# Performance work log

Hardware: AMD Instinct MI355X
Metric: run time of the kernel (lower is better)

Reference implementation:

```python
import jax, jax.numpy as jnp
import numpy as np
import math

VOCAB = 32000
D_MODEL = 64
N_LAYERS = 4
B, S = 512, 1000
EPS = 1e-5


def _layer_norm(x, g, b):
    mu = jnp.mean(x, axis=-1, keepdims=True)
    var = jnp.mean(jnp.square(x - mu), axis=-1, keepdims=True)
    return (x - mu) * jax.lax.rsqrt(var + EPS) * g + b


def _pos_encoding(seq_len, d_model, dtype):
    pos = jnp.arange(seq_len, dtype=dtype)[:, None]                      # [S,1]
    div = jnp.exp(jnp.arange(0, d_model, 2, dtype=dtype) * (-math.log(10000.0) / d_model))  # [d/2]
    ang = pos * div                                                       # [S,d/2]
    pe = jnp.stack([jnp.sin(ang), jnp.cos(ang)], axis=-1).reshape(seq_len, d_model)
    return pe  # [S,d]


def setup_inputs() -> dict:
    key = jax.random.key(0)
    ks = jax.random.split(key, 14)
    d, L = D_MODEL, N_LAYERS
    sc = 0.05
    return {
        "tokens": jax.random.randint(ks[0], (B, S), 0, VOCAB, dtype=jnp.int64 if jax.config.jax_enable_x64 else jnp.int32),
        "emb":   jax.random.normal(ks[1], (VOCAB, d), jnp.float32) * sc,
        "lin_w": jax.random.normal(ks[2], (L, d, d), jnp.float32) * sc,   # [out,in] per layer
        "lin_b": jnp.zeros((L, d), jnp.float32),
        "ff1_w": jax.random.normal(ks[3], (L, d, d), jnp.float32) * sc,
        "ff1_b": jnp.zeros((L, d), jnp.float32),
        "ff2_w": jax.random.normal(ks[4], (L, d, d), jnp.float32) * sc,
        "ff2_b": jnp.zeros((L, d), jnp.float32),
        "n1_g":  jnp.ones((L, d), jnp.float32),
        "n1_b":  jnp.zeros((L, d), jnp.float32),
        "n2_g":  jnp.ones((L, d), jnp.float32),
        "n2_b":  jnp.zeros((L, d), jnp.float32),
        "out_w": jax.random.normal(ks[5], (2, d), jnp.float32) * sc,
        "out_b": jnp.zeros((2,), jnp.float32),
    }


def reference(tokens, emb, lin_w, lin_b, ff1_w, ff1_b, ff2_w, ff2_b,
              n1_g, n1_b, n2_g, n2_b, out_w, out_b):
    d = emb.shape[1]
    x = emb[tokens] * jnp.asarray(math.sqrt(d), emb.dtype)               # [B,S,d]
    x = x + _pos_encoding(tokens.shape[1], d, x.dtype)[None, :, :]
    # dropout is identity in eval mode
    for l in range(lin_w.shape[0]):
        avg = jnp.mean(x, axis=1, keepdims=True)                          # [B,1,d]
        attn = jnp.einsum('bkd,od->bko', avg, lin_w[l]) + lin_b[l]        # [B,1,d], broadcasts
        x = _layer_norm(x + attn, n1_g[l], n1_b[l])
        h = jax.nn.relu(jnp.einsum('bsd,od->bso', x, ff1_w[l]) + ff1_b[l])
        h = jnp.einsum('bsd,od->bso', h, ff2_w[l]) + ff2_b[l]
        x = _layer_norm(x + h, n2_g[l], n2_b[l])
    logits = jnp.einsum('bsd,od->bso', x, out_w) + out_b                  # [B,S,2]
    return logits
```

## Files before the change

### kernel.cpp

```cpp
#include <hip/hip_runtime.h>
#include <stdint.h>

#define TPB 1024
#define NL 4

typedef _Float16 f16;
typedef _Float16 half2v __attribute__((ext_vector_type(2)));
typedef _Float16 f16x8 __attribute__((ext_vector_type(8)));
typedef float f32x4 __attribute__((ext_vector_type(4)));
typedef uint32_t u32x2 __attribute__((ext_vector_type(2)));
typedef uint32_t u32x4 __attribute__((ext_vector_type(4)));

#define XIU(r, c) ((r) * 32 + (((((c) >> 2) ^ ((r) & 7))) << 2) + ((c) & 3))

static __device__ __forceinline__ uint32_t packh2(float a, float b) {
  half2v h;
  h.x = (_Float16)a;
  h.y = (_Float16)b;
  return __builtin_bit_cast(uint32_t, h);
}
static __device__ __forceinline__ float2 unpackh2(uint32_t u) {
  half2v h = __builtin_bit_cast(half2v, u);
  return make_float2((float)h.x, (float)h.y);
}

__global__ void pack_weights_kernel(const float* __restrict__ ff1_w,
                                    const float* __restrict__ ff2_w,
                                    f16* __restrict__ w1h,
                                    f16* __restrict__ w2h,
                                    float* __restrict__ petab) {
  int idx = blockIdx.x * blockDim.x + threadIdx.x;
  if (idx < 16384) {
    w1h[idx] = (f16)ff1_w[idx];
  } else if (idx < 32768) {
    w2h[idx - 16384] = (f16)ff2_w[idx - 16384];
  } else if (petab != nullptr && idx < 32768 + 64000) {
    int j = idx - 32768;
    int s = j >> 6, d = j & 63;
    float div = exp2f(-0.4152410118609203f * (float)(d >> 1));
    float ang = (float)s * div;
    petab[j] = (d & 1) ? cosf(ang) : sinf(ang);
  }
}

__global__ __launch_bounds__(TPB) void aat_kernel(
    const int* __restrict__ tokens, const float* __restrict__ emb,
    const float* __restrict__ lin_w, const float* __restrict__ lin_b,
    const float* __restrict__ ff1_b, const float* __restrict__ ff2_b,
    const float* __restrict__ n1_g, const float* __restrict__ n1_b,
    const float* __restrict__ n2_g, const float* __restrict__ n2_b,
    const float* __restrict__ out_w, const float* __restrict__ out_b,
    const f16* __restrict__ w1h, const f16* __restrict__ w2h,
    const float* __restrict__ petab, float* __restrict__ out) {
  __shared__ __align__(16) uint32_t X2[1024 * 32];
  __shared__ __align__(16) uint32_t Hreg[256 * 32];

  const int t = threadIdx.x;
  const int b = blockIdx.x;
  const int lane = t & 63;
  const int wv = t >> 6;
  const bool valid = (t < 1000);
  float* redbuf = (float*)Hreg;
  float* avgbuf = (float*)(Hreg + 2048);
  float* attnbuf = (float*)(Hreg + 2112);

  if (valid) {
    int tok = tokens[b * 1000 + t];
    const float4* ev = (const float4*)(emb + (size_t)tok * 64);
    const int r7 = t & 7;
    if (petab != nullptr) {
      const float4* pv = (const float4*)(petab + (size_t)t * 64);
      #pragma unroll
      for (int q = 0; q < 8; q++) {
        float4 v0 = ev[2 * q], v1 = ev[2 * q + 1];
        float4 p0 = pv[2 * q], p1 = pv[2 * q + 1];
        u32x4 w;
        w[0] = packh2(fmaf(v0.x, 8.f, p0.x), fmaf(v0.y, 8.f, p0.y));
        w[1] = packh2(fmaf(v0.z, 8.f, p0.z), fmaf(v0.w, 8.f, p0.w));
        w[2] = packh2(fmaf(v1.x, 8.f, p1.x), fmaf(v1.y, 8.f, p1.y));
        w[3] = packh2(fmaf(v1.z, 8.f, p1.z), fmaf(v1.w, 8.f, p1.w));
        *(u32x4*)(&X2[t * 32 + ((q ^ r7) << 2)]) = w;
      }
    } else {
      float fs = (float)t;
      #pragma unroll
      for (int q = 0; q < 8; q++) {
        float4 v0 = ev[2 * q], v1 = ev[2 * q + 1];
        float d0 = exp2f(-0.4152410118609203f * (float)(4 * q));
        float d1 = exp2f(-0.4152410118609203f * (float)(4 * q + 1));
        float d2 = exp2f(-0.4152410118609203f * (float)(4 * q + 2));
        float d3 = exp2f(-0.4152410118609203f * (float)(4 * q + 3));
        u32x4 w;
        w[0] = packh2(fmaf(v0.x, 8.f, sinf(fs * d0)), fmaf(v0.y, 8.f, cosf(fs * d0)));
        w[1] = packh2(fmaf(v0.z, 8.f, sinf(fs * d1)), fmaf(v0.w, 8.f, cosf(fs * d1)));
        w[2] = packh2(fmaf(v1.x, 8.f, sinf(fs * d2)), fmaf(v1.y, 8.f, cosf(fs * d2)));
        w[3] = packh2(fmaf(v1.z, 8.f, sinf(fs * d3)), fmaf(v1.w, 8.f, cosf(fs * d3)));
        *(u32x4*)(&X2[t * 32 + ((q ^ r7) << 2)]) = w;
      }
    }
  } else {
    #pragma unroll
    for (int c = 0; c < 32; c += 4)
      *(u32x4*)(&X2[t * 32 + c]) = (u32x4){0u, 0u, 0u, 0u};
  }
  __syncthreads();

  const int l15 = lane & 15;
  const int g4 = lane >> 4;
  const int e7 = l15 & 7;
  const int nt = wv & 3;
  const int mr = wv >> 2;
  const int cw = 8 * nt + 2 * g4;
  const int cswz = (((cw >> 2) ^ e7) << 2) + (cw & 3);

  #pragma unroll 1
  for (int l = 0; l < NL; l++) {
    const float* n1g = n1_g + l * 64;
    const float* n1b = n1_b + l * 64;
    const float* n2gl = n2_g + l * 64;
    const float* n2bl = n2_b + l * 64;

    const f16* w1p = w1h + l * 4096 + (16 * nt + l15) * 64 + 8 * g4;
    f16x8 A10 = *(const f16x8*)(w1p);
    f16x8 A11 = *(const f16x8*)(w1p + 32);
    const f16* w2p = w2h + l * 4096 + (16 * nt + l15) * 64 + 8 * g4;
    f16x8 A20 = *(const f16x8*)(w2p);
    f16x8 A21 = *(const f16x8*)(w2p + 32);
    f32x4 bias1 = *(const f32x4*)(ff1_b + l * 64 + 16 * nt + 4 * g4);
    f32x4 bias2 = *(const f32x4*)(ff2_b + l * 64 + 16 * nt + 4 * g4);

    {
      int cp = t & 31, rg = t >> 5;
      float s0 = 0.f, s1 = 0.f;
      for (int r = rg; r < 1000; r += 32) {
        float2 v = unpackh2(X2[XIU(r, cp)]);
        s0 += v.x;
        s1 += v.y;
      }
      redbuf[rg * 64 + 2 * cp] = s0;
      redbuf[rg * 64 + 2 * cp + 1] = s1;
    }
    __syncthreads();
    if (t < 64) {
      float ssum = 0.f;
      #pragma unroll
      for (int w = 0; w < 32; w++) ssum += redbuf[w * 64 + t];
      avgbuf[t] = ssum * 1e-3f;
    }
    if (t < 64) {
      const float* wr = lin_w + (size_t)(l * 64 + t) * 64;
      float a0 = lin_b[l * 64 + t], a1 = 0.f, a2 = 0.f, a3 = 0.f;
      #pragma unroll
      for (int d = 0; d < 64; d += 4) {
        a0 += avgbuf[d] * wr[d];
        a1 += avgbuf[d + 1] * wr[d + 1];
        a2 += avgbuf[d + 2] * wr[d + 2];
        a3 += avgbuf[d + 3] * wr[d + 3];
      }
      attnbuf[t] = (a0 + a1) + (a2 + a3);
    }
    __syncthreads();

    if (valid) {
      const float2* at2 = (const float2*)attnbuf;
      const int r7 = t & 7;
      float m0 = 0.f, q0 = 0.f;
      #pragma unroll
      for (int q = 0; q < 8; q++) {
        u32x4 w = *(const u32x4*)(&X2[t * 32 + ((q ^ r7) << 2)]);
        #pragma unroll
        for (int j = 0; j < 4; j++) {
          float2 xv = unpackh2(w[j]);
          float2 at = at2[q * 4 + j];
          float a0 = xv.x + at.x, a1 = xv.y + at.y;
          m0 += a0 + a1;
          q0 = fmaf(a0, a0, q0);
          q0 = fmaf(a1, a1, q0);
        }
      }
      float mu = m0 * (1.0f / 64.0f);
      float var = q0 * (1.0f / 64.0f) - mu * mu;
      float rs = rsqrtf(var + 1e-5f);
      #pragma unroll
      for (int q = 0; q < 8; q++) {
        u32x4 w = *(const u32x4*)(&X2[t * 32 + ((q ^ r7) << 2)]);
        u32x4 o;
        #pragma unroll
        for (int j = 0; j < 4; j++) {
          float2 xv = unpackh2(w[j]);
          float2 at = at2[q * 4 + j];
          int d = (q * 4 + j) * 2;
          float a0 = xv.x + at.x, a1 = xv.y + at.y;
          o[j] = packh2(fmaf((a0 - mu) * rs, n1g[d], n1b[d]),
                        fmaf((a1 - mu) * rs, n1g[d + 1], n1b[d + 1]));
        }
        *(u32x4*)(&X2[t * 32 + ((q ^ r7) << 2)]) = o;
      }
    }
    __syncthreads();

    #pragma unroll 1
    for (int i = 0; i < 4; i++) {
      const int s0 = 256 * i + 64 * mr;
      #pragma unroll 2
      for (int sb = 0; sb < 4; sb++) {
        const int s = s0 + 16 * sb + l15;
        u32x4 b0 = *(const u32x4*)(&X2[s * 32 + ((g4 ^ e7) << 2)]);
        u32x4 b1 = *(const u32x4*)(&X2[s * 32 + (((4 + g4) ^ e7) << 2)]);
        f32x4 acc = bias1;
        acc = __builtin_amdgcn_mfma_f32_16x16x32_f16(
            A10, __builtin_bit_cast(f16x8, b0), acc, 0, 0, 0);
        acc = __builtin_amdgcn_mfma_f32_16x16x32_f16(
            A11, __builtin_bit_cast(f16x8, b1), acc, 0, 0, 0);
        const int hr = 64 * mr + 16 * sb + l15;
        u32x2 hp;
        hp[0] = packh2(fmaxf(acc[0], 0.f), fmaxf(acc[1], 0.f));
        hp[1] = packh2(fmaxf(acc[2], 0.f), fmaxf(acc[3], 0.f));
        *(u32x2*)(&Hreg[hr * 32 + cswz]) = hp;
      }
      __syncthreads();
      #pragma unroll 2
      for (int sb = 0; sb < 4; sb++) {
        const int s = s0 + 16 * sb + l15;
        const int hr = 64 * mr + 16 * sb + l15;
        u32x4 h0 = *(const u32x4*)(&Hreg[hr * 32 + ((g4 ^ e7) << 2)]);
        u32x4 h1 = *(const u32x4*)(&Hreg[hr * 32 + (((4 + g4) ^ e7) << 2)]);
        u32x2 ry = *(const u32x2*)(&X2[s * 32 + cswz]);
        float2 r0 = unpackh2(ry[0]), r1 = unpackh2(ry[1]);
        f32x4 acc = bias2;
        acc[0] += r0.x;
        acc[1] += r0.y;
        acc[2] += r1.x;
        acc[3] += r1.y;
        acc = __builtin_amdgcn_mfma_f32_16x16x32_f16(
            A20, __builtin_bit_cast(f16x8, h0), acc, 0, 0, 0);
        acc = __builtin_amdgcn_mfma_f32_16x16x32_f16(
            A21, __builtin_bit_cast(f16x8, h1), acc, 0, 0, 0);
        u32x2 tw;
        tw[0] = packh2(acc[0], acc[1]);
        tw[1] = packh2(acc[2], acc[3]);
        *(u32x2*)(&X2[s * 32 + cswz]) = tw;
      }
      __syncthreads();
    }

    if (valid) {
      const int r7 = t & 7;
      float m0 = 0.f, q0 = 0.f;
      #pragma unroll
      for (int q = 0; q < 8; q++) {
        u32x4 w = *(const u32x4*)(&X2[t * 32 + ((q ^ r7) << 2)]);
        #pragma unroll
        for (int j = 0; j < 4; j++) {
          float2 tv = unpackh2(w[j]);
          m0 += tv.x + tv.y;
          q0 = fmaf(tv.x, tv.x, q0);
          q0 = fmaf(tv.y, tv.y, q0);
        }
      }
      float mu2 = m0 * (1.0f / 64.0f);
      float var2 = q0 * (1.0f / 64.0f) - mu2 * mu2;
      float rs2 = rsqrtf(var2 + 1e-5f);
      #pragma unroll
      for (int q = 0; q < 8; q++) {
        u32x4 w = *(const u32x4*)(&X2[t * 32 + ((q ^ r7) << 2)]);
        u32x4 o;
        #pragma unroll
        for (int j = 0; j < 4; j++) {
          float2 tv = unpackh2(w[j]);
          int d = (q * 4 + j) * 2;
          o[j] = packh2(fmaf((tv.x - mu2) * rs2, n2gl[d], n2bl[d]),
                        fmaf((tv.y - mu2) * rs2, n2gl[d + 1], n2bl[d + 1]));
        }
        *(u32x4*)(&X2[t * 32 + ((q ^ r7) << 2)]) = o;
      }
    } else {
      #pragma unroll
      for (int c = 0; c < 32; c += 4)
        *(u32x4*)(&X2[t * 32 + c]) = (u32x4){0u, 0u, 0u, 0u};
    }
    __syncthreads();
  }

  if (valid) {
    const int r7 = t & 7;
    float a0 = out_b[0], a1 = out_b[1];
    #pragma unroll
    for (int q = 0; q < 8; q++) {
      u32x4 w = *(const u32x4*)(&X2[t * 32 + ((q ^ r7) << 2)]);
      #pragma unroll
      for (int j = 0; j < 4; j++) {
        float2 xv = unpackh2(w[j]);
        int d = (q * 4 + j) * 2;
        a0 += xv.x * out_w[d] + xv.y * out_w[d + 1];
        a1 += xv.x * out_w[64 + d] + xv.y * out_w[64 + d + 1];
      }
    }
    *(float2*)(out + (size_t)(b * 1000 + t) * 2) = make_float2(a0, a1);
  }
}

extern "C" void kernel_launch(void* const* d_in, const int* in_sizes, int n_in,
                              void* d_out, int out_size, void* d_ws, size_t ws_size,
                              hipStream_t stream) {
  const int* tokens = (const int*)d_in[0];
  const float* emb = (const float*)d_in[1];
  const float* lin_w = (const float*)d_in[2];
  const float* lin_b = (const float*)d_in[3];
  const float* ff1_w = (const float*)d_in[4];
  const float* ff1_b = (const float*)d_in[5];
  const float* ff2_w = (const float*)d_in[6];
  const float* ff2_b = (const float*)d_in[7];
  const float* n1_g = (const float*)d_in[8];
  const float* n1_b = (const float*)d_in[9];
  const float* n2_g = (const float*)d_in[10];
  const float* n2_b = (const float*)d_in[11];
  const float* out_w = (const float*)d_in[12];
  const float* out_b = (const float*)d_in[13];
  float* out = (float*)d_out;

  f16* w1h = (f16*)d_ws;
  f16* w2h = w1h + 16384;
  float* petab = (float*)((char*)d_ws + 65536);
  const size_t need = 65536 + 64000 * 4;
  const bool use_pe = (ws_size >= need);
  float* pe_arg = use_pe ? petab : nullptr;

  int pack_threads = 32768 + (use_pe ? 64000 : 0);
  int pack_blocks = (pack_threads + 255) / 256;
  pack_weights_kernel<<<pack_blocks, 256, 0, stream>>>(ff1_w, ff2_w, w1h, w2h, pe_arg);
  aat_kernel<<<512, TPB, 0, stream>>>(tokens, emb, lin_w, lin_b, ff1_b, ff2_b,
                                      n1_g, n1_b, n2_g, n2_b, out_w, out_b,
                                      w1h, w2h, pe_arg, out);
}
```

Baseline: 280.8 us.

## Double-buffer FFN hidden tile to overlap GEMM1 and GEMM2 with fewer barriers

Splits the FFN over 1024 rows into 8 chunks of 128 rows and double-buffers the hidden activations in shared memory. The first GEMM of chunk c now runs alongside the second GEMM of chunk c-1, with a single barrier per chunk instead of two per 256-row slab. The layer-norm passes also keep the row in registers instead of re-reading shared memory. This adds register pressure and a scheduling barrier, and the row mapping changes per wave.

Result: slower. 309.1 us (+10.1%).

```diff
diff --git a/kernel.cpp b/kernel.cpp
--- a/kernel.cpp
+++ b/kernel.cpp
@@ -53,16 +53,16 @@
     const f16* __restrict__ w1h, const f16* __restrict__ w2h,
     const float* __restrict__ petab, float* __restrict__ out) {
   __shared__ __align__(16) uint32_t X2[1024 * 32];
-  __shared__ __align__(16) uint32_t Hreg[256 * 32];
+  __shared__ __align__(16) uint32_t Hb[2 * 4096];
 
   const int t = threadIdx.x;
   const int b = blockIdx.x;
   const int lane = t & 63;
   const int wv = t >> 6;
   const bool valid = (t < 1000);
-  float* redbuf = (float*)Hreg;
-  float* avgbuf = (float*)(Hreg + 2048);
-  float* attnbuf = (float*)(Hreg + 2112);
+  float* redbuf = (float*)Hb;
+  float* avgbuf = (float*)(Hb + 2048);
+  float* attnbuf = (float*)(Hb + 2112);
 
   if (valid) {
     int tok = tokens[b * 1000 + t];
@@ -164,116 +164,111 @@
     if (valid) {
       const float2* at2 = (const float2*)attnbuf;
       const int r7 = t & 7;
+      u32x4 wq0 = *(const u32x4*)(&X2[t * 32 + ((0 ^ r7) << 2)]);
+      u32x4 wq1 = *(const u32x4*)(&X2[t * 32 + ((1 ^ r7) << 2)]);
+      u32x4 wq2 = *(const u32x4*)(&X2[t * 32 + ((2 ^ r7) << 2)]);
+      u32x4 wq3 = *(const u32x4*)(&X2[t * 32 + ((3 ^ r7) << 2)]);
+      u32x4 wq4 = *(const u32x4*)(&X2[t * 32 + ((4 ^ r7) << 2)]);
+      u32x4 wq5 = *(const u32x4*)(&X2[t * 32 + ((5 ^ r7) << 2)]);
+      u32x4 wq6 = *(const u32x4*)(&X2[t * 32 + ((6 ^ r7) << 2)]);
+      u32x4 wq7 = *(const u32x4*)(&X2[t * 32 + ((7 ^ r7) << 2)]);
       float m0 = 0.f, q0 = 0.f;
-      #pragma unroll
-      for (int q = 0; q < 8; q++) {
-        u32x4 w = *(const u32x4*)(&X2[t * 32 + ((q ^ r7) << 2)]);
-        #pragma unroll
-        for (int j = 0; j < 4; j++) {
-          float2 xv = unpackh2(w[j]);
-          float2 at = at2[q * 4 + j];
-          float a0 = xv.x + at.x, a1 = xv.y + at.y;
-          m0 += a0 + a1;
-          q0 = fmaf(a0, a0, q0);
-          q0 = fmaf(a1, a1, q0);
-        }
-      }
+#define LN1S(WQ, Q) { _Pragma("unroll") for (int j = 0; j < 4; j++) { \
+      float2 xv = unpackh2(WQ[j]); float2 at = at2[(Q) * 4 + j]; \
+      float a0 = xv.x + at.x, a1 = xv.y + at.y; \
+      m0 += a0 + a1; q0 = fmaf(a0, a0, q0); q0 = fmaf(a1, a1, q0); } }
+      LN1S(wq0, 0) LN1S(wq1, 1) LN1S(wq2, 2) LN1S(wq3, 3)
+      LN1S(wq4, 4) LN1S(wq5, 5) LN1S(wq6, 6) LN1S(wq7, 7)
+#undef LN1S
       float mu = m0 * (1.0f / 64.0f);
       float var = q0 * (1.0f / 64.0f) - mu * mu;
       float rs = rsqrtf(var + 1e-5f);
-      #pragma unroll
-      for (int q = 0; q < 8; q++) {
-        u32x4 w = *(const u32x4*)(&X2[t * 32 + ((q ^ r7) << 2)]);
-        u32x4 o;
-        #pragma unroll
-        for (int j = 0; j < 4; j++) {
-          float2 xv = unpackh2(w[j]);
-          float2 at = at2[q * 4 + j];
-          int d = (q * 4 + j) * 2;
-          float a0 = xv.x + at.x, a1 = xv.y + at.y;
-          o[j] = packh2(fmaf((a0 - mu) * rs, n1g[d], n1b[d]),
-                        fmaf((a1 - mu) * rs, n1g[d + 1], n1b[d + 1]));
-        }
-        *(u32x4*)(&X2[t * 32 + ((q ^ r7) << 2)]) = o;
-      }
-    }
-    __syncthreads();
-
+#define LN1N(WQ, Q) { u32x4 o; _Pragma("unroll") for (int j = 0; j < 4; j++) { \
+      float2 xv = unpackh2(WQ[j]); float2 at = at2[(Q) * 4 + j]; \
+      int d = ((Q) * 4 + j) * 2; \
+      float a0 = xv.x + at.x, a1 = xv.y + at.y; \
+      o[j] = packh2(fmaf((a0 - mu) * rs, n1g[d], n1b[d]), \
+                    fmaf((a1 - mu) * rs, n1g[d + 1], n1b[d + 1])); } \
+      *(u32x4*)(&X2[t * 32 + (((Q) ^ r7) << 2)]) = o; }
+      LN1N(wq0, 0) LN1N(wq1, 1) LN1N(wq2, 2) LN1N(wq3, 3)
+      LN1N(wq4, 4) LN1N(wq5, 5) LN1N(wq6, 6) LN1N(wq7, 7)
+#undef LN1N
+    }
+    __syncthreads();
+
+#define MM1C(C, HB) { _Pragma("unroll") for (int sb = 0; sb < 2; sb++) { \
+    const int s = 128 * (C) + 32 * mr + 16 * sb + l15; \
+    u32x4 b0 = *(const u32x4*)(&X2[s * 32 + ((g4 ^ e7) << 2)]); \
+    u32x4 b1 = *(const u32x4*)(&X2[s * 32 + (((4 + g4) ^ e7) << 2)]); \
+    f32x4 acc = bias1; \
+    acc = __builtin_amdgcn_mfma_f32_16x16x32_f16(A10, __builtin_bit_cast(f16x8, b0), acc, 0, 0, 0); \
+    acc = __builtin_amdgcn_mfma_f32_16x16x32_f16(A11, __builtin_bit_cast(f16x8, b1), acc, 0, 0, 0); \
+    const int hr = 32 * mr + 16 * sb + l15; \
+    u32x2 hp; \
+    hp[0] = packh2(fmaxf(acc[0], 0.f), fmaxf(acc[1], 0.f)); \
+    hp[1] = packh2(fmaxf(acc[2], 0.f), fmaxf(acc[3], 0.f)); \
+    *(u32x2*)(&(HB)[hr * 32 + cswz]) = hp; } }
+
+#define MM2C(C, HB) { _Pragma("unroll") for (int sb = 0; sb < 2; sb++) { \
+    const int s = 128 * (C) + 32 * mr + 16 * sb + l15; \
+    const int hr = 32 * mr + 16 * sb + l15; \
+    u32x4 h0 = *(const u32x4*)(&(HB)[hr * 32 + ((g4 ^ e7) << 2)]); \
+    u32x4 h1 = *(const u32x4*)(&(HB)[hr * 32 + (((4 + g4) ^ e7) << 2)]); \
+    u32x2 ry = *(const u32x2*)(&X2[s * 32 + cswz]); \
+    float2 r0 = unpackh2(ry[0]), r1 = unpackh2(ry[1]); \
+    f32x4 acc = bias2; \
+    acc[0] += r0.x; acc[1] += r0.y; acc[2] += r1.x; acc[3] += r1.y; \
+    acc = __builtin_amdgcn_mfma_f32_16x16x32_f16(A20, __builtin_bit_cast(f16x8, h0), acc, 0, 0, 0); \
+    acc = __builtin_amdgcn_mfma_f32_16x16x32_f16(A21, __builtin_bit_cast(f16x8, h1), acc, 0, 0, 0); \
+    u32x2 tw; \
+    tw[0] = packh2(acc[0], acc[1]); \
+    tw[1] = packh2(acc[2], acc[3]); \
+    *(u32x2*)(&X2[s * 32 + cswz]) = tw; } }
+
+    MM1C(0, Hb)
+    __syncthreads();
     #pragma unroll 1
-    for (int i = 0; i < 4; i++) {
-      const int s0 = 256 * i + 64 * mr;
-      #pragma unroll 2
-      for (int sb = 0; sb < 4; sb++) {
-        const int s = s0 + 16 * sb + l15;
-        u32x4 b0 = *(const u32x4*)(&X2[s * 32 + ((g4 ^ e7) << 2)]);
-        u32x4 b1 = *(const u32x4*)(&X2[s * 32 + (((4 + g4) ^ e7) << 2)]);
-        f32x4 acc = bias1;
-        acc = __builtin_amdgcn_mfma_f32_16x16x32_f16(
-            A10, __builtin_bit_cast(f16x8, b0), acc, 0, 0, 0);
-        acc = __builtin_amdgcn_mfma_f32_16x16x32_f16(
-            A11, __builtin_bit_cast(f16x8, b1), acc, 0, 0, 0);
-        const int hr = 64 * mr + 16 * sb + l15;
-        u32x2 hp;
-        hp[0] = packh2(fmaxf(acc[0], 0.f), fmaxf(acc[1], 0.f));
-        hp[1] = packh2(fmaxf(acc[2], 0.f), fmaxf(acc[3], 0.f));
-        *(u32x2*)(&Hreg[hr * 32 + cswz]) = hp;
-      }
+    for (int c = 1; c < 8; c++) {
+      uint32_t* cur = Hb + ((c & 1) << 12);
+      uint32_t* prv = Hb + (((c - 1) & 1) << 12);
+      MM1C(c, cur)
+      __builtin_amdgcn_sched_barrier(0);
+      MM2C(c - 1, prv)
       __syncthreads();
-      #pragma unroll 2
-      for (int sb = 0; sb < 4; sb++) {
-        const int s = s0 + 16 * sb + l15;
-        const int hr = 64 * mr + 16 * sb + l15;
-        u32x4 h0 = *(const u32x4*)(&Hreg[hr * 32 + ((g4 ^ e7) << 2)]);
-        u32x4 h1 = *(const u32x4*)(&Hreg[hr * 32 + (((4 + g4) ^ e7) << 2)]);
-        u32x2 ry = *(const u32x2*)(&X2[s * 32 + cswz]);
-        float2 r0 = unpackh2(ry[0]), r1 = unpackh2(ry[1]);
-        f32x4 acc = bias2;
-        acc[0] += r0.x;
-        acc[1] += r0.y;
-        acc[2] += r1.x;
-        acc[3] += r1.y;
-        acc = __builtin_amdgcn_mfma_f32_16x16x32_f16(
-            A20, __builtin_bit_cast(f16x8, h0), acc, 0, 0, 0);
-        acc = __builtin_amdgcn_mfma_f32_16x16x32_f16(
-            A21, __builtin_bit_cast(f16x8, h1), acc, 0, 0, 0);
-        u32x2 tw;
-        tw[0] = packh2(acc[0], acc[1]);
-        tw[1] = packh2(acc[2], acc[3]);
-        *(u32x2*)(&X2[s * 32 + cswz]) = tw;
-      }
-      __syncthreads();
-    }
+    }
+    MM2C(7, Hb + 4096)
+    __syncthreads();
+#undef MM1C
+#undef MM2C
 
     if (valid) {
       const int r7 = t & 7;
+      u32x4 wq0 = *(const u32x4*)(&X2[t * 32 + ((0 ^ r7) << 2)]);
+      u32x4 wq1 = *(const u32x4*)(&X2[t * 32 + ((1 ^ r7) << 2)]);
+      u32x4 wq2 = *(const u32x4*)(&X2[t * 32 + ((2 ^ r7) << 2)]);
+      u32x4 wq3 = *(const u32x4*)(&X2[t * 32 + ((3 ^ r7) << 2)]);
+      u32x4 wq4 = *(const u32x4*)(&X2[t * 32 + ((4 ^ r7) << 2)]);
+      u32x4 wq5 = *(const u32x4*)(&X2[t * 32 + ((5 ^ r7) << 2)]);
+      u32x4 wq6 = *(const u32x4*)(&X2[t * 32 + ((6 ^ r7) << 2)]);
+      u32x4 wq7 = *(const u32x4*)(&X2[t * 32 + ((7 ^ r7) << 2)]);
       float m0 = 0.f, q0 = 0.f;
-      #pragma unroll
-      for (int q = 0; q < 8; q++) {
-        u32x4 w = *(const u32x4*)(&X2[t * 32 + ((q ^ r7) << 2)]);
-        #pragma unroll
-        for (int j = 0; j < 4; j++) {
-          float2 tv = unpackh2(w[j]);
-          m0 += tv.x + tv.y;
-          q0 = fmaf(tv.x, tv.x, q0);
-          q0 = fmaf(tv.y, tv.y, q0);
-        }
-      }
+#define LN2S(WQ) { _Pragma("unroll") for (int j = 0; j < 4; j++) { \
+      float2 tv = unpackh2(WQ[j]); \
+      m0 += tv.x + tv.y; q0 = fmaf(tv.x, tv.x, q0); q0 = fmaf(tv.y, tv.y, q0); } }
+      LN2S(wq0) LN2S(wq1) LN2S(wq2) LN2S(wq3)
+      LN2S(wq4) LN2S(wq5) LN2S(wq6) LN2S(wq7)
+#undef LN2S
       float mu2 = m0 * (1.0f / 64.0f);
       float var2 = q0 * (1.0f / 64.0f) - mu2 * mu2;
       float rs2 = rsqrtf(var2 + 1e-5f);
-      #pragma unroll
-      for (int q = 0; q < 8; q++) {
-        u32x4 w = *(const u32x4*)(&X2[t * 32 + ((q ^ r7) << 2)]);
-        u32x4 o;
-        #pragma unroll
-        for (int j = 0; j < 4; j++) {
-          float2 tv = unpackh2(w[j]);
-          int d = (q * 4 + j) * 2;
-          o[j] = packh2(fmaf((tv.x - mu2) * rs2, n2gl[d], n2bl[d]),
-                        fmaf((tv.y - mu2) * rs2, n2gl[d + 1], n2bl[d + 1]));
-        }
-        *(u32x4*)(&X2[t * 32 + ((q ^ r7) << 2)]) = o;
-      }
+#define LN2N(WQ, Q) { u32x4 o; _Pragma("unroll") for (int j = 0; j < 4; j++) { \
+      float2 tv = unpackh2(WQ[j]); int d = ((Q) * 4 + j) * 2; \
+      o[j] = packh2(fmaf((tv.x - mu2) * rs2, n2gl[d], n2bl[d]), \
+                    fmaf((tv.y - mu2) * rs2, n2gl[d + 1], n2bl[d + 1])); } \
+      *(u32x4*)(&X2[t * 32 + (((Q) ^ r7) << 2)]) = o; }
+      LN2N(wq0, 0) LN2N(wq1, 1) LN2N(wq2, 2) LN2N(wq3, 3)
+      LN2N(wq4, 4) LN2N(wq5, 5) LN2N(wq6, 6) LN2N(wq7, 7)
+#undef LN2N
     } else {
       #pragma unroll
       for (int c = 0; c < 32; c += 4)
```

## Double-buffer hidden activations to overlap FF1 and FF2 across sequence chunks

Applied to the files above, without the earlier changes.

Replaces the four-chunk FF1/FF2 loop, which needed two barriers per chunk, with eight smaller 128-row chunks using two ping-pong H buffers. Each iteration computes FF1 for chunk c and FF2 for chunk c-1 with a single barrier between iterations, halving barrier count per chunk and letting MFMA work from the two stages interleave. Shared memory use stays the same size, but each MFMA phase now has less work per barrier, and a sched_barrier restricts compiler reordering.

New measurement: 280.9 us. About the same (+0.0%).

```diff
diff --git a/kernel.cpp b/kernel.cpp
--- a/kernel.cpp
+++ b/kernel.cpp
@@ -53,16 +53,16 @@
     const f16* __restrict__ w1h, const f16* __restrict__ w2h,
     const float* __restrict__ petab, float* __restrict__ out) {
   __shared__ __align__(16) uint32_t X2[1024 * 32];
-  __shared__ __align__(16) uint32_t Hreg[256 * 32];
+  __shared__ __align__(16) uint32_t Hb[2 * 4096];
 
   const int t = threadIdx.x;
   const int b = blockIdx.x;
   const int lane = t & 63;
   const int wv = t >> 6;
   const bool valid = (t < 1000);
-  float* redbuf = (float*)Hreg;
-  float* avgbuf = (float*)(Hreg + 2048);
-  float* attnbuf = (float*)(Hreg + 2112);
+  float* redbuf = (float*)Hb;
+  float* avgbuf = (float*)(Hb + 2048);
+  float* attnbuf = (float*)(Hb + 2112);
 
   if (valid) {
     int tok = tokens[b * 1000 + t];
@@ -199,50 +199,50 @@
     }
     __syncthreads();
 
+#define MM1C(C, HB) { _Pragma("unroll") for (int sb = 0; sb < 2; sb++) { \
+    const int s = 128 * (C) + 32 * mr + 16 * sb + l15; \
+    u32x4 b0 = *(const u32x4*)(&X2[s * 32 + ((g4 ^ e7) << 2)]); \
+    u32x4 b1 = *(const u32x4*)(&X2[s * 32 + (((4 + g4) ^ e7) << 2)]); \
+    f32x4 acc = bias1; \
+    acc = __builtin_amdgcn_mfma_f32_16x16x32_f16(A10, __builtin_bit_cast(f16x8, b0), acc, 0, 0, 0); \
+    acc = __builtin_amdgcn_mfma_f32_16x16x32_f16(A11, __builtin_bit_cast(f16x8, b1), acc, 0, 0, 0); \
+    const int hr = 32 * mr + 16 * sb + l15; \
+    u32x2 hp; \
+    hp[0] = packh2(fmaxf(acc[0], 0.f), fmaxf(acc[1], 0.f)); \
+    hp[1] = packh2(fmaxf(acc[2], 0.f), fmaxf(acc[3], 0.f)); \
+    *(u32x2*)(&(HB)[hr * 32 + cswz]) = hp; } }
+
+#define MM2C(C, HB) { _Pragma("unroll") for (int sb = 0; sb < 2; sb++) { \
+    const int s = 128 * (C) + 32 * mr + 16 * sb + l15; \
+    const int hr = 32 * mr + 16 * sb + l15; \
+    u32x4 h0 = *(const u32x4*)(&(HB)[hr * 32 + ((g4 ^ e7) << 2)]); \
+    u32x4 h1 = *(const u32x4*)(&(HB)[hr * 32 + (((4 + g4) ^ e7) << 2)]); \
+    u32x2 ry = *(const u32x2*)(&X2[s * 32 + cswz]); \
+    float2 r0 = unpackh2(ry[0]), r1 = unpackh2(ry[1]); \
+    f32x4 acc = bias2; \
+    acc[0] += r0.x; acc[1] += r0.y; acc[2] += r1.x; acc[3] += r1.y; \
+    acc = __builtin_amdgcn_mfma_f32_16x16x32_f16(A20, __builtin_bit_cast(f16x8, h0), acc, 0, 0, 0); \
+    acc = __builtin_amdgcn_mfma_f32_16x16x32_f16(A21, __builtin_bit_cast(f16x8, h1), acc, 0, 0, 0); \
+    u32x2 tw; \
+    tw[0] = packh2(acc[0], acc[1]); \
+    tw[1] = packh2(acc[2], acc[3]); \
+    *(u32x2*)(&X2[s * 32 + cswz]) = tw; } }
+
+    MM1C(0, Hb)
+    __syncthreads();
     #pragma unroll 1
-    for (int i = 0; i < 4; i++) {
-      const int s0 = 256 * i + 64 * mr;
-      #pragma unroll 2
-      for (int sb = 0; sb < 4; sb++) {
-        const int s = s0 + 16 * sb + l15;
-        u32x4 b0 = *(const u32x4*)(&X2[s * 32 + ((g4 ^ e7) << 2)]);
-        u32x4 b1 = *(const u32x4*)(&X2[s * 32 + (((4 + g4) ^ e7) << 2)]);
-        f32x4 acc = bias1;
-        acc = __builtin_amdgcn_mfma_f32_16x16x32_f16(
-            A10, __builtin_bit_cast(f16x8, b0), acc, 0, 0, 0);
-        acc = __builtin_amdgcn_mfma_f32_16x16x32_f16(
-            A11, __builtin_bit_cast(f16x8, b1), acc, 0, 0, 0);
-        const int hr = 64 * mr + 16 * sb + l15;
-        u32x2 hp;
-        hp[0] = packh2(fmaxf(acc[0], 0.f), fmaxf(acc[1], 0.f));
-        hp[1] = packh2(fmaxf(acc[2], 0.f), fmaxf(acc[3], 0.f));
-        *(u32x2*)(&Hreg[hr * 32 + cswz]) = hp;
-      }
+    for (int c = 1; c < 8; c++) {
+      uint32_t* cur = Hb + ((c & 1) << 12);
+      uint32_t* prv = Hb + (((c - 1) & 1) << 12);
+      MM1C(c, cur)
+      __builtin_amdgcn_sched_barrier(0);
+      MM2C(c - 1, prv)
       __syncthreads();
-      #pragma unroll 2
-      for (int sb = 0; sb < 4; sb++) {
-        const int s = s0 + 16 * sb + l15;
-        const int hr = 64 * mr + 16 * sb + l15;
-        u32x4 h0 = *(const u32x4*)(&Hreg[hr * 32 + ((g4 ^ e7) << 2)]);
-        u32x4 h1 = *(const u32x4*)(&Hreg[hr * 32 + (((4 + g4) ^ e7) << 2)]);
-        u32x2 ry = *(const u32x2*)(&X2[s * 32 + cswz]);
-        float2 r0 = unpackh2(ry[0]), r1 = unpackh2(ry[1]);
-        f32x4 acc = bias2;
-        acc[0] += r0.x;
-        acc[1] += r0.y;
-        acc[2] += r1.x;
-        acc[3] += r1.y;
-        acc = __builtin_amdgcn_mfma_f32_16x16x32_f16(
-            A20, __builtin_bit_cast(f16x8, h0), acc, 0, 0, 0);
-        acc = __builtin_amdgcn_mfma_f32_16x16x32_f16(
-            A21, __builtin_bit_cast(f16x8, h1), acc, 0, 0, 0);
-        u32x2 tw;
-        tw[0] = packh2(acc[0], acc[1]);
-        tw[1] = packh2(acc[2], acc[3]);
-        *(u32x2*)(&X2[s * 32 + cswz]) = tw;
-      }
-      __syncthreads();
-    }
+    }
+    MM2C(7, Hb + 4096)
+    __syncthreads();
+#undef MM1C
+#undef MM2C
 
     if (valid) {
       const int r7 = t & 7;
```
